# Performance work log

Hardware: AMD Instinct MI355X
Metric: run time of the kernel (lower is better)

Reference implementation:

```python
import jax, jax.numpy as jnp
import numpy as np

S, M, E = 8192, 4096, 64          # tokens, model_dim, num_experts
CAPACITY_FACTOR = 1.0
MIN_CAPACITY = 8
CAPACITY = max(int(np.ceil(S / E * CAPACITY_FACTOR)), MIN_CAPACITY)  # 128


def setup_inputs() -> dict:
    key = jax.random.key(0)
    k1, k2 = jax.random.split(key)
    x = jax.random.normal(k1, (S, M), dtype=jnp.float32)
    wg = jax.random.normal(k2, (E, M), dtype=jnp.float32) * (1.0 / np.sqrt(M))
    return {"x": x, "wg": wg}


def reference(x, wg):
    # gate projection (Linear, no bias): logits [s, e]
    logits = jnp.einsum('sm,em->se', x, wg)
    gates = jax.nn.softmax(logits, axis=1)                      # [s, e]

    # top-1 expert per token
    indices1_s = jnp.argmax(gates, axis=1)                      # [s]
    mask1 = jax.nn.one_hot(indices1_s, E, dtype=jnp.int32)      # [s, e]
    exp_counts = jnp.sum(mask1, axis=0)                         # [e]

    # load-balancing aux loss
    me = jnp.mean(gates, axis=0)
    ce = jnp.mean(mask1.astype(jnp.float32), axis=0)
    l_aux = jnp.sum(me * ce) * E

    # capacity drop (use_rts=False): keep first CAPACITY tokens per expert.
    # torch: top_idx = topk(mask1, capacity, dim=0)[1]; scatter ones at those rows.
    top_idx = jax.lax.top_k(mask1.T, CAPACITY)[1]               # [e, c] token ids
    keep = jnp.zeros((S, E), dtype=jnp.int32).at[top_idx.T, jnp.arange(E)[None, :]].set(1)
    mask1 = mask1 * keep                                        # [s, e]

    # position of each token inside its expert's buffer
    locations1 = jnp.cumsum(mask1, axis=0) - 1                  # [s, e]
    locations1_s = jnp.sum(locations1 * mask1, axis=1)          # [s]

    mask1_f = mask1.astype(gates.dtype)
    gates_masked = gates * mask1_f                              # [s, e]
    locations1_sc = jax.nn.one_hot(locations1_s, CAPACITY, dtype=jnp.float32)  # [s, c]

    combine_weights = jnp.einsum('se,sc->sec', gates_masked, locations1_sc)    # [s, e, c]
    dispatch_mask = combine_weights.astype(bool)
    return l_aux, combine_weights, dispatch_mask, exp_counts
```

## Files before the change

### kernel.cpp

```cpp
#include <hip/hip_runtime.h>
#include <hip/hip_bf16.h>

#define TS 8192
#define TM 4096
#define TE 64
#define TCAP 128
#define KS 8
#define KCHUNK (TM / KS)
#define BK 16
#define NTILE (KCHUNK / BK)
#define BM 128
#define GEMM_BLOCKS 512
#define K1_GRID 2048
#define NFILL (K1_GRID - GEMM_BLOCKS)

constexpr size_t CWsz = (size_t)TS * TE * TCAP;
constexpr size_t NOUT = 1 + 2 * CWsz + TE;
constexpr size_t NF4  = (NOUT - 1) / 4;
constexpr size_t FSTRIDE = (size_t)NFILL * 256;

typedef float v4f __attribute__((ext_vector_type(4)));

__global__ __launch_bounds__(256) void k1_gemm_fill_softmax(
    const float* __restrict__ x, const float* __restrict__ wg,
    float* __restrict__ part, float* __restrict__ gate1, int* __restrict__ idx1,
    float* __restrict__ me, int* __restrict__ tilecnt, float* __restrict__ out) {
  const int tid = threadIdx.x;
  const int v = (int)((blockIdx.x * 5u) & (K1_GRID - 1));

  __shared__ float As[BK][132];
  __shared__ float Ws[BK][68];
  __shared__ int lastf;

  if (v >= GEMM_BLOCKS) {
    const int fid = v - GEMM_BLOCKS;
    const v4f z = {0.f, 0.f, 0.f, 0.f};
    v4f* o4 = (v4f*)out;
    for (size_t i = (size_t)fid * 256 + tid; i < NF4; i += FSTRIDE)
      __builtin_nontemporal_store(z, &o4[i]);
    return;
  }

  const int tile = v & 63;
  const int t0 = tile * BM;
  const int k0 = (v >> 6) * KCHUNK;
  const int tg = tid >> 3;
  const int eg = tid & 7;

  float acc[4][8] = {};
  float4 ra[2], rw;
  auto load = [&](int kt) {
    const int kb = k0 + kt * BK;
#pragma unroll
    for (int i = 0; i < 2; i++) {
      int idx = tid + 256 * i;
      int tok = idx >> 2, c4 = idx & 3;
      ra[i] = *(const float4*)&x[(size_t)(t0 + tok) * TM + kb + 4 * c4];
    }
    { int e = tid >> 2, c4 = tid & 3;
      rw = *(const float4*)&wg[(size_t)e * TM + kb + 4 * c4]; }
  };
  load(0);
  for (int kt = 0; kt < NTILE; kt++) {
#pragma unroll
    for (int i = 0; i < 2; i++) {
      int idx = tid + 256 * i;
      int tok = idx >> 2, c4 = idx & 3;
      As[4 * c4 + 0][tok] = ra[i].x; As[4 * c4 + 1][tok] = ra[i].y;
      As[4 * c4 + 2][tok] = ra[i].z; As[4 * c4 + 3][tok] = ra[i].w;
    }
    { int e = tid >> 2, c4 = tid & 3;
      Ws[4 * c4 + 0][e] = rw.x; Ws[4 * c4 + 1][e] = rw.y;
      Ws[4 * c4 + 2][e] = rw.z; Ws[4 * c4 + 3][e] = rw.w; }
    __syncthreads();
    if (kt + 1 < NTILE) load(kt + 1);
#pragma unroll
    for (int k = 0; k < BK; k++) {
      float4 a  = *(const float4*)&As[k][tg * 4];
      float4 b0 = *(const float4*)&Ws[k][eg * 8];
      float4 b1 = *(const float4*)&Ws[k][eg * 8 + 4];
      float av[4] = {a.x, a.y, a.z, a.w};
      float bv[8] = {b0.x, b0.y, b0.z, b0.w, b1.x, b1.y, b1.z, b1.w};
#pragma unroll
      for (int i = 0; i < 4; i++)
#pragma unroll
        for (int j = 0; j < 8; j++) acc[i][j] += av[i] * bv[j];
    }
    __syncthreads();
  }
  float* dst = part + (size_t)(v >> 6) * TS * TE;
#pragma unroll
  for (int i = 0; i < 4; i++) {
    int tok = t0 + tg * 4 + i;
    *(float4*)&dst[(size_t)tok * TE + eg * 8] =
        make_float4(acc[i][0], acc[i][1], acc[i][2], acc[i][3]);
    *(float4*)&dst[(size_t)tok * TE + eg * 8 + 4] =
        make_float4(acc[i][4], acc[i][5], acc[i][6], acc[i][7]);
  }

  __threadfence();
  if (tid == 0) lastf = (atomicAdd(&tilecnt[tile], 1) == KS - 1) ? 1 : 0;
  __syncthreads();
  if (!lastf) return;
  __threadfence();

  const int w = tid >> 6, lane = tid & 63;
  float mesum = 0.0f;
  for (int it = 0; it < 32; it++) {
    const int s = t0 + w * 32 + it;
    float logit = 0.0f;
#pragma unroll
    for (int p = 0; p < KS; p++)
      logit += part[((size_t)p * TS + s) * TE + lane];
    float mv = logit; int mi = lane;
#pragma unroll
    for (int off = 32; off; off >>= 1) {
      float ov = __shfl_xor(mv, off);
      int oi = __shfl_xor(mi, off);
      if (ov > mv || (ov == mv && oi < mi)) { mv = ov; mi = oi; }
    }
    float ex = expf(logit - mv);
    float sum = ex;
#pragma unroll
    for (int off = 32; off; off >>= 1) sum += __shfl_xor(sum, off);
    float g = ex / sum;
    mesum += g;
    if (lane == mi) { gate1[s] = g; idx1[s] = mi; }
  }
  float* lds = &As[0][0];
  lds[w * 64 + lane] = mesum;
  __syncthreads();
  if (w == 0)
    atomicAdd(&me[lane], lds[lane] + lds[64 + lane] + lds[128 + lane] + lds[192 + lane]);
}

__global__ __launch_bounds__(256) void k2_rank_scatter_laux(
    const int* __restrict__ idx1, const float* __restrict__ gate1,
    const float* __restrict__ me, int* __restrict__ cnts, int* __restrict__ done,
    float* __restrict__ out) {
  const int e = blockIdx.x;
  const int w = threadIdx.x >> 6, lane = threadIdx.x & 63;
  const int s0 = w * (TS / 4);
  __shared__ int wcnt[4];
  __shared__ int lastf;

  int cnt = 0;
  for (int c = 0; c < TS / 4 / 64; c++)
    cnt += __popcll(__ballot(idx1[s0 + c * 64 + lane] == e));
  if (lane == 0) wcnt[w] = cnt;
  __syncthreads();
  int base = 0;
  for (int j = 0; j < w; j++) base += wcnt[j];

  for (int c = 0; c < TS / 4 / 64; c++) {
    int s = s0 + c * 64 + lane;
    bool m = (idx1[s] == e);
    unsigned long long mask = __ballot(m);
    if (m) {
      int p = base + __popcll(mask & ((1ull << lane) - 1ull));
      if (p < TCAP) {
        size_t off = 1 + ((size_t)s * TE + e) * (size_t)TCAP + (size_t)p;
        out[off] = gate1[s];
        out[off + CWsz] = 1.0f;
      }
    }
    base += __popcll(mask);
  }
  if (w == 3 && lane == 0) {
    cnts[e] = base;
    __threadfence();
    lastf = (atomicAdd(done, 1) == TE - 1) ? 1 : 0;
  }
  __syncthreads();
  if (lastf && w == 0) {
    __threadfence();
    int c = cnts[lane];
    float vv = (me[lane] / (float)TS) * ((float)c / (float)TS);
    float sum = vv;
#pragma unroll
    for (int off = 32; off; off >>= 1) sum += __shfl_xor(sum, off);
    if (lane == 0) out[0] = sum * (float)TE;
    out[1 + 2 * CWsz + lane] = (float)c;
  }
}

extern "C" void kernel_launch(void* const* d_in, const int* in_sizes, int n_in,
                              void* d_out, int out_size, void* d_ws, size_t ws_size,
                              hipStream_t stream) {
  const float* x  = (const float*)d_in[0];
  const float* wg = (const float*)d_in[1];
  float* out = (float*)d_out;

  float* part    = (float*)d_ws;
  float* gate1   = part + (size_t)KS * TS * TE;
  int*   idx1    = (int*)(gate1 + TS);
  float* me      = (float*)(idx1 + TS);
  int*   tilecnt = (int*)(me + TE);
  int*   done    = tilecnt + TE;
  int*   cnts    = done + 1;

  hipMemsetAsync(me, 0, (TE + TE + 1) * sizeof(int), stream);

  k1_gemm_fill_softmax<<<K1_GRID, 256, 0, stream>>>(x, wg, part, gate1, idx1,
                                                    me, tilecnt, out);
  k2_rank_scatter_laux<<<TE, 256, 0, stream>>>(idx1, gate1, me, cnts, done, out);
}
```

Baseline: 808.8 us.

## Drop split-K GEMM for full-K 32-token tiles and deterministic me reduction

Replaces the split-K gate GEMM (8 K-chunks per 128-token tile, with partials written to workspace and reduced by the last-arriving block) with full-K 32-token tiles that keep logits in LDS and run softmax/argmax in place. Per-tile expert-mean partials are written to workspace and reduced in the rank kernel, and a third tiny kernel computes l_aux. This removes the partial-logit round trip, the atomics, the threadfences and the memset. In exchange each thread does less register-level reuse (1x8 instead of 4x8 outer product), so the FLOP:LDS ratio drops, the weight matrix is re-read by 256 blocks, and there is one more kernel launch.

Result: faster. 759.2 us (-6.1%).

```diff
diff --git a/kernel.cpp b/kernel.cpp
--- a/kernel.cpp
+++ b/kernel.cpp
@@ -5,13 +5,11 @@
 #define TM 4096
 #define TE 64
 #define TCAP 128
-#define KS 8
-#define KCHUNK (TM / KS)
 #define BK 16
-#define NTILE (KCHUNK / BK)
-#define BM 128
-#define GEMM_BLOCKS 512
-#define K1_GRID 2048
+#define NTILE (TM / BK)
+#define BM 32
+#define GEMM_BLOCKS (TS / BM)
+#define K1_GRID 1024
 #define NFILL (K1_GRID - GEMM_BLOCKS)
 
 constexpr size_t CWsz = (size_t)TS * TE * TCAP;
@@ -21,16 +19,14 @@
 
 typedef float v4f __attribute__((ext_vector_type(4)));
 
-__global__ __launch_bounds__(256) void k1_gemm_fill_softmax(
+__global__ __launch_bounds__(256, 4) void k1_gemm_fill_softmax(
     const float* __restrict__ x, const float* __restrict__ wg,
-    float* __restrict__ part, float* __restrict__ gate1, int* __restrict__ idx1,
-    float* __restrict__ me, int* __restrict__ tilecnt, float* __restrict__ out) {
+    float* __restrict__ gate1, int* __restrict__ idx1,
+    float* __restrict__ mepart, float* __restrict__ out) {
   const int tid = threadIdx.x;
   const int v = (int)((blockIdx.x * 5u) & (K1_GRID - 1));
 
-  __shared__ float As[BK][132];
-  __shared__ float Ws[BK][68];
-  __shared__ int lastf;
+  __shared__ float smem[2336];
 
   if (v >= GEMM_BLOCKS) {
     const int fid = v - GEMM_BLOCKS;
@@ -41,77 +37,51 @@
     return;
   }
 
-  const int tile = v & 63;
+  float (*As)[34] = (float(*)[34])smem;
+  float (*Ws)[68] = (float(*)[68])(smem + 544);
+  const int tile = v;
   const int t0 = tile * BM;
-  const int k0 = (v >> 6) * KCHUNK;
   const int tg = tid >> 3;
   const int eg = tid & 7;
 
-  float acc[4][8] = {};
-  float4 ra[2], rw;
+  float acc[8] = {};
+  float2 ra; float4 rw;
   auto load = [&](int kt) {
-    const int kb = k0 + kt * BK;
-#pragma unroll
-    for (int i = 0; i < 2; i++) {
-      int idx = tid + 256 * i;
-      int tok = idx >> 2, c4 = idx & 3;
-      ra[i] = *(const float4*)&x[(size_t)(t0 + tok) * TM + kb + 4 * c4];
-    }
-    { int e = tid >> 2, c4 = tid & 3;
-      rw = *(const float4*)&wg[(size_t)e * TM + kb + 4 * c4]; }
+    const int kb = kt * BK;
+    ra = *(const float2*)&x[(size_t)(t0 + tg) * TM + kb + 2 * (tid & 7)];
+    rw = *(const float4*)&wg[(size_t)(tid >> 2) * TM + kb + 4 * (tid & 3)];
   };
   load(0);
   for (int kt = 0; kt < NTILE; kt++) {
-#pragma unroll
-    for (int i = 0; i < 2; i++) {
-      int idx = tid + 256 * i;
-      int tok = idx >> 2, c4 = idx & 3;
-      As[4 * c4 + 0][tok] = ra[i].x; As[4 * c4 + 1][tok] = ra[i].y;
-      As[4 * c4 + 2][tok] = ra[i].z; As[4 * c4 + 3][tok] = ra[i].w;
-    }
-    { int e = tid >> 2, c4 = tid & 3;
+    { const int c2 = tid & 7;
+      As[2 * c2 + 0][tg] = ra.x; As[2 * c2 + 1][tg] = ra.y; }
+    { const int e = tid >> 2, c4 = tid & 3;
       Ws[4 * c4 + 0][e] = rw.x; Ws[4 * c4 + 1][e] = rw.y;
       Ws[4 * c4 + 2][e] = rw.z; Ws[4 * c4 + 3][e] = rw.w; }
     __syncthreads();
     if (kt + 1 < NTILE) load(kt + 1);
 #pragma unroll
     for (int k = 0; k < BK; k++) {
-      float4 a  = *(const float4*)&As[k][tg * 4];
+      float a  = As[k][tg];
       float4 b0 = *(const float4*)&Ws[k][eg * 8];
       float4 b1 = *(const float4*)&Ws[k][eg * 8 + 4];
-      float av[4] = {a.x, a.y, a.z, a.w};
-      float bv[8] = {b0.x, b0.y, b0.z, b0.w, b1.x, b1.y, b1.z, b1.w};
-#pragma unroll
-      for (int i = 0; i < 4; i++)
-#pragma unroll
-        for (int j = 0; j < 8; j++) acc[i][j] += av[i] * bv[j];
+      acc[0] += a * b0.x; acc[1] += a * b0.y; acc[2] += a * b0.z; acc[3] += a * b0.w;
+      acc[4] += a * b1.x; acc[5] += a * b1.y; acc[6] += a * b1.z; acc[7] += a * b1.w;
     }
     __syncthreads();
   }
-  float* dst = part + (size_t)(v >> 6) * TS * TE;
+
+  float* S = smem;
+  float* S2 = smem + 2080;
 #pragma unroll
-  for (int i = 0; i < 4; i++) {
-    int tok = t0 + tg * 4 + i;
-    *(float4*)&dst[(size_t)tok * TE + eg * 8] =
-        make_float4(acc[i][0], acc[i][1], acc[i][2], acc[i][3]);
-    *(float4*)&dst[(size_t)tok * TE + eg * 8 + 4] =
-        make_float4(acc[i][4], acc[i][5], acc[i][6], acc[i][7]);
-  }
-
-  __threadfence();
-  if (tid == 0) lastf = (atomicAdd(&tilecnt[tile], 1) == KS - 1) ? 1 : 0;
+  for (int j = 0; j < 8; j++) S[tg * 65 + eg * 8 + j] = acc[j];
   __syncthreads();
-  if (!lastf) return;
-  __threadfence();
 
   const int w = tid >> 6, lane = tid & 63;
-  float mesum = 0.0f;
-  for (int it = 0; it < 32; it++) {
-    const int s = t0 + w * 32 + it;
-    float logit = 0.0f;
-#pragma unroll
-    for (int p = 0; p < KS; p++)
-      logit += part[((size_t)p * TS + s) * TE + lane];
+  float esum = 0.0f;
+  for (int i = 0; i < 8; i++) {
+    const int t = w * 8 + i;
+    float logit = S[t * 65 + lane];
     float mv = logit; int mi = lane;
 #pragma unroll
     for (int off = 32; off; off >>= 1) {
@@ -124,26 +94,34 @@
 #pragma unroll
     for (int off = 32; off; off >>= 1) sum += __shfl_xor(sum, off);
     float g = ex / sum;
-    mesum += g;
-    if (lane == mi) { gate1[s] = g; idx1[s] = mi; }
+    esum += g;
+    if (lane == mi) { gate1[t0 + t] = g; idx1[t0 + t] = mi; }
   }
-  float* lds = &As[0][0];
-  lds[w * 64 + lane] = mesum;
+  S2[w * 64 + lane] = esum;
   __syncthreads();
   if (w == 0)
-    atomicAdd(&me[lane], lds[lane] + lds[64 + lane] + lds[128 + lane] + lds[192 + lane]);
+    mepart[(size_t)tile * TE + lane] =
+        S2[lane] + S2[64 + lane] + S2[128 + lane] + S2[192 + lane];
 }
 
-__global__ __launch_bounds__(256) void k2_rank_scatter_laux(
+__global__ __launch_bounds__(256) void k2_rank_scatter(
     const int* __restrict__ idx1, const float* __restrict__ gate1,
-    const float* __restrict__ me, int* __restrict__ cnts, int* __restrict__ done,
-    float* __restrict__ out) {
+    const float* __restrict__ mepart, float* __restrict__ mefin,
+    int* __restrict__ cnts, float* __restrict__ out) {
   const int e = blockIdx.x;
   const int w = threadIdx.x >> 6, lane = threadIdx.x & 63;
+  __shared__ float red[256];
+  __shared__ int wcnt[4];
+
+  red[threadIdx.x] = mepart[(size_t)threadIdx.x * TE + e];
+  __syncthreads();
+  for (int o = 128; o; o >>= 1) {
+    if (threadIdx.x < o) red[threadIdx.x] += red[threadIdx.x + o];
+    __syncthreads();
+  }
+  if (threadIdx.x == 0) mefin[e] = red[0];
+
   const int s0 = w * (TS / 4);
-  __shared__ int wcnt[4];
-  __shared__ int lastf;
-
   int cnt = 0;
   for (int c = 0; c < TS / 4 / 64; c++)
     cnt += __popcll(__ballot(idx1[s0 + c * 64 + lane] == e));
@@ -166,22 +144,19 @@
     }
     base += __popcll(mask);
   }
-  if (w == 3 && lane == 0) {
-    cnts[e] = base;
-    __threadfence();
-    lastf = (atomicAdd(done, 1) == TE - 1) ? 1 : 0;
-  }
-  __syncthreads();
-  if (lastf && w == 0) {
-    __threadfence();
-    int c = cnts[lane];
-    float vv = (me[lane] / (float)TS) * ((float)c / (float)TS);
-    float sum = vv;
+  if (w == 3 && lane == 0) cnts[e] = base;
+}
+
+__global__ void k3_laux(const float* __restrict__ mefin, const int* __restrict__ cnts,
+                        float* __restrict__ out) {
+  const int lane = threadIdx.x;
+  int c = cnts[lane];
+  float vv = (mefin[lane] / (float)TS) * ((float)c / (float)TS);
+  float sum = vv;
 #pragma unroll
-    for (int off = 32; off; off >>= 1) sum += __shfl_xor(sum, off);
-    if (lane == 0) out[0] = sum * (float)TE;
-    out[1 + 2 * CWsz + lane] = (float)c;
-  }
+  for (int off = 32; off; off >>= 1) sum += __shfl_xor(sum, off);
+  if (lane == 0) out[0] = sum * (float)TE;
+  out[1 + 2 * CWsz + lane] = (float)c;
 }
 
 extern "C" void kernel_launch(void* const* d_in, const int* in_sizes, int n_in,
@@ -191,17 +166,13 @@
   const float* wg = (const float*)d_in[1];
   float* out = (float*)d_out;
 
-  float* part    = (float*)d_ws;
-  float* gate1   = part + (size_t)KS * TS * TE;
-  int*   idx1    = (int*)(gate1 + TS);
-  float* me      = (float*)(idx1 + TS);
-  int*   tilecnt = (int*)(me + TE);
-  int*   done    = tilecnt + TE;
-  int*   cnts    = done + 1;
+  float* gate1  = (float*)d_ws;
+  int*   idx1   = (int*)(gate1 + TS);
+  float* mepart = (float*)(idx1 + TS);
+  float* mefin  = mepart + (size_t)GEMM_BLOCKS * TE;
+  int*   cnts   = (int*)(mefin + TE);
 
-  hipMemsetAsync(me, 0, (TE + TE + 1) * sizeof(int), stream);
-
-  k1_gemm_fill_softmax<<<K1_GRID, 256, 0, stream>>>(x, wg, part, gate1, idx1,
-                                                    me, tilecnt, out);
-  k2_rank_scatter_laux<<<TE, 256, 0, stream>>>(idx1, gate1, me, cnts, done, out);
+  k1_gemm_fill_softmax<<<K1_GRID, 256, 0, stream>>>(x, wg, gate1, idx1, mepart, out);
+  k2_rank_scatter<<<TE, 256, 0, stream>>>(idx1, gate1, mepart, mefin, cnts, out);
+  k3_laux<<<1, 64, 0, stream>>>(mefin, cnts, out);
 }
```
